# Kernel tuning notes

Measured on AMD Instinct MI355X. Metric: run time of the kernel, lower is better.

The kernel has to match this reference:

```python
import jax, jax.numpy as jnp
import numpy as np
import math

B, S, E, H, F, L, V = 4, 256, 512, 8, 2048, 4, 32000
HD = E // H
MAXLEN = 5000  # EnhancedPositionalEncoding max_len default


def _ln(x, s, b):
    m = jnp.mean(x, axis=-1, keepdims=True)
    v = jnp.mean((x - m) ** 2, axis=-1, keepdims=True)
    return (x - m) / jnp.sqrt(v + 1e-5) * s + b


def setup_inputs() -> dict:
    key = jax.random.key(0)
    ks = jax.random.split(key, 10)
    n = lambda k, shape: jax.random.normal(k, shape, jnp.float32) * 0.02
    return {
        "src": jax.random.randint(ks[0], (B, S), 0, V),
        "emb": jax.random.uniform(ks[1], (V, E), jnp.float32, -0.1, 0.1),
        "rel_table": n(ks[2], (2 * MAXLEN - 1, E)),
        "norm_in_s": jnp.ones(E, jnp.float32), "norm_in_b": jnp.zeros(E, jnp.float32),
        "inW": n(ks[3], (L, 3 * E, E)), "inB": jnp.zeros((L, 3 * E), jnp.float32),
        "outW": n(ks[4], (L, E, E)), "outB": jnp.zeros((L, E), jnp.float32),
        "ln1_s": jnp.ones((L, E), jnp.float32), "ln1_b": jnp.zeros((L, E), jnp.float32),
        "ln2_s": jnp.ones((L, E), jnp.float32), "ln2_b": jnp.zeros((L, E), jnp.float32),
        "w1": n(ks[5], (L, F, E)), "b1": jnp.zeros((L, F), jnp.float32),
        "w2": n(ks[6], (L, E, F)), "b2": jnp.zeros((L, E), jnp.float32),
        "normf_s": jnp.ones(E, jnp.float32), "normf_b": jnp.zeros(E, jnp.float32),
        "dec_w": jax.random.uniform(ks[7], (V, E), jnp.float32, -0.1, 0.1),
        "dec_b": jnp.zeros(V, jnp.float32),
    }


def reference(src, emb, rel_table, norm_in_s, norm_in_b, inW, inB, outW, outB,
              ln1_s, ln1_b, ln2_s, ln2_b, w1, b1, w2, b2, normf_s, normf_b,
              dec_w, dec_b):
    x = emb[src] * math.sqrt(E)                 # [B,S,E], pos_encoder is identity in relative mode
    x = _ln(x, norm_in_s, norm_in_b)
    # relative-position embedding gather: idx[l,m] = (m - l) + S - 1
    pos = jnp.arange(S)
    rel_idx = (pos[None, :] - pos[:, None]) + S - 1
    rel = rel_table[rel_idx].reshape(S, S, H, HD)  # [S,S,H,hd]
    # NOTE: torch adds the BOOL triu mask to float scores -> +1.0 at masked positions
    mask = jnp.triu(jnp.ones((S, S), jnp.float32), 1)
    scale = 1.0 / math.sqrt(HD)
    for l in range(L):
        h = _ln(x, ln1_s[l], ln1_b[l])
        qkv = h @ inW[l].T + inB[l]
        q, k, v = jnp.split(qkv, 3, axis=-1)
        q = q.reshape(B, S, H, HD).transpose(0, 2, 1, 3)  # [B,H,S,hd]
        k = k.reshape(B, S, H, HD).transpose(0, 2, 1, 3)
        v = v.reshape(B, S, H, HD).transpose(0, 2, 1, 3)
        scores = jnp.einsum('bhqd,bhkd->bhqk', q, k) * scale
        bias = jnp.einsum('bhld,lmhd->bhlm', q, rel)      # relative-position bias (unscaled, as in torch)
        attn = jax.nn.softmax(scores + bias + mask, axis=-1)
        o = jnp.einsum('bhqk,bhkd->bhqd', attn, v).transpose(0, 2, 1, 3).reshape(B, S, E)
        x = x + (o @ outW[l].T + outB[l])
        h2 = _ln(x, ln2_s[l], ln2_b[l])
        ff = jax.nn.gelu(h2 @ w1[l].T + b1[l], approximate=False) @ w2[l].T + b2[l]
        x = x + ff
    x = _ln(x, normf_s, normf_b)  # encoder final norm
    return x @ dec_w.T + dec_b    # [B,S,V]
```

## Files before the change

### kernel.cpp

```cpp
#include <hip/hip_runtime.h>
#include <hip/hip_bf16.h>
#include <math.h>

#define BB 4
#define SS 256
#define EE 512
#define HH 8
#define HD 64
#define FFD 2048
#define LL 4
#define VV 32000
#define BS (BB*SS)
#define SQRT_E 22.627416997969522f
#define ATTN_SCALE 0.125f

typedef __bf16 bf16;
typedef __attribute__((ext_vector_type(4))) __bf16 bf16x4;
typedef __attribute__((ext_vector_type(8))) __bf16 bf16x8;
typedef __attribute__((ext_vector_type(4))) float f32x4;

#define GLOBAL_AS __attribute__((address_space(1)))
#define LDS_AS    __attribute__((address_space(3)))

__device__ __forceinline__ void load_lds16(const bf16* g, bf16* l) {
    __builtin_amdgcn_global_load_lds((const GLOBAL_AS unsigned int*)g,
                                     (LDS_AS unsigned int*)l, 16, 0, 0);
}

__global__ void cvt_all(const float* __restrict__ inW, const float* __restrict__ outW,
                        const float* __restrict__ w1, const float* __restrict__ w2,
                        const float* __restrict__ dec, const float* __restrict__ rel,
                        bf16* __restrict__ inWb, bf16* __restrict__ outWb,
                        bf16* __restrict__ w1b, bf16* __restrict__ w2b,
                        bf16* __restrict__ decb, bf16* __restrict__ relb,
                        const int* __restrict__ src, const float* __restrict__ emb,
                        const float* __restrict__ nsc, const float* __restrict__ nbi,
                        float* __restrict__ xout) {
    int b = blockIdx.x;
    int t = threadIdx.x;
    if (b >= 28544) {
        int row = b - 28544;
        const float* r = emb + (size_t)src[row] * EE;
        float v0 = r[t] * SQRT_E, v1 = r[t + 256] * SQRT_E;
        float sum = v0 + v1, sq = v0 * v0 + v1 * v1;
        #pragma unroll
        for (int off = 32; off; off >>= 1) {
            sum += __shfl_xor(sum, off);
            sq  += __shfl_xor(sq, off);
        }
        __shared__ float ssum[4], ssq[4];
        int wid = t >> 6, lane = t & 63;
        if (lane == 0) { ssum[wid] = sum; ssq[wid] = sq; }
        __syncthreads();
        sum = ssum[0] + ssum[1] + ssum[2] + ssum[3];
        sq  = ssq[0] + ssq[1] + ssq[2] + ssq[3];
        float mean = sum * (1.0f / EE);
        float var  = sq * (1.0f / EE) - mean * mean;
        float rstd = rsqrtf(var + 1e-5f);
        xout[(size_t)row * EE + t]       = (v0 - mean) * rstd * nsc[t] + nbi[t];
        xout[(size_t)row * EE + t + 256] = (v1 - mean) * rstd * nsc[t + 256] + nbi[t + 256];
        return;
    }
    const float* s; bf16* d; int base; int n;
    if (b < 3072)       { s = inW;  d = inWb;  base = b;         n = 3145728; }
    else if (b < 4096)  { s = outW; d = outWb; base = b - 3072;  n = 1048576; }
    else if (b < 8192)  { s = w1;   d = w1b;   base = b - 4096;  n = 4194304; }
    else if (b < 12288) { s = w2;   d = w2b;   base = b - 8192;  n = 4194304; }
    else if (b < 28288) { s = dec;  d = decb;  base = b - 12288; n = 16384000; }
    else                { s = rel;  d = relb;  base = b - 28288; n = 261632; }
    int i = (base * 256 + t) * 4;
    if (i < n) {
        float4 v = *(const float4*)(s + i);
        bf16x4 o;
        o[0] = (bf16)v.x; o[1] = (bf16)v.y; o[2] = (bf16)v.z; o[3] = (bf16)v.w;
        *(bf16x4*)(d + i) = o;
    }
}

template <typename OT>
__global__ void ln_kernel(const float* __restrict__ in, const float* __restrict__ sc,
                          const float* __restrict__ bi, OT* __restrict__ out) {
    int row = blockIdx.x;
    int t = threadIdx.x;
    const float* r = in + (size_t)row * EE;
    float v0 = r[t], v1 = r[t + 256];
    float sum = v0 + v1, sq = v0 * v0 + v1 * v1;
    #pragma unroll
    for (int off = 32; off; off >>= 1) {
        sum += __shfl_xor(sum, off);
        sq  += __shfl_xor(sq, off);
    }
    __shared__ float ssum[4], ssq[4];
    int wid = t >> 6, lane = t & 63;
    if (lane == 0) { ssum[wid] = sum; ssq[wid] = sq; }
    __syncthreads();
    sum = ssum[0] + ssum[1] + ssum[2] + ssum[3];
    sq  = ssq[0] + ssq[1] + ssq[2] + ssq[3];
    float mean = sum * (1.0f / EE);
    float var  = sq * (1.0f / EE) - mean * mean;
    float rstd = rsqrtf(var + 1e-5f);
    out[(size_t)row * EE + t]       = (OT)((v0 - mean) * rstd * sc[t] + bi[t]);
    out[(size_t)row * EE + t + 256] = (OT)((v1 - mean) * rstd * sc[t + 256] + bi[t + 256]);
}

__global__ void embed_ln_kernel(const int* __restrict__ src, const float* __restrict__ emb,
                                const float* __restrict__ sc, const float* __restrict__ bi,
                                float* __restrict__ out) {
    int row = blockIdx.x;
    int t = threadIdx.x;
    const float* r = emb + (size_t)src[row] * EE;
    float v0 = r[t] * SQRT_E, v1 = r[t + 256] * SQRT_E;
    float sum = v0 + v1, sq = v0 * v0 + v1 * v1;
    #pragma unroll
    for (int off = 32; off; off >>= 1) {
        sum += __shfl_xor(sum, off);
        sq  += __shfl_xor(sq, off);
    }
    __shared__ float ssum[4], ssq[4];
    int wid = t >> 6, lane = t & 63;
    if (lane == 0) { ssum[wid] = sum; ssq[wid] = sq; }
    __syncthreads();
    sum = ssum[0] + ssum[1] + ssum[2] + ssum[3];
    sq  = ssq[0] + ssq[1] + ssq[2] + ssq[3];
    float mean = sum * (1.0f / EE);
    float var  = sq * (1.0f / EE) - mean * mean;
    float rstd = rsqrtf(var + 1e-5f);
    out[(size_t)row * EE + t]       = (v0 - mean) * rstd * sc[t] + bi[t];
    out[(size_t)row * EE + t + 256] = (v1 - mean) * rstd * sc[t + 256] + bi[t + 256];
}

template <int BM, int BN, int MODE, int OBF16, int WRVT, int SWZ, int SPLITK>
__global__ __launch_bounds__(256) void gemm_bf16(
        const bf16* __restrict__ A, const bf16* __restrict__ W,
        const float* __restrict__ bias, void* __restrict__ Cout,
        const float* __restrict__ res, bf16* __restrict__ vT,
        int M, int N, int K) {
    constexpr int FM = BM / 32, FN = BN / 32;
    __shared__ bf16 Atile[2][BM * 32];
    __shared__ bf16 Btile[2][BN * 32];
    int tid = threadIdx.x;
    int wid = tid >> 6, lane = tid & 63;
    int wm = (wid >> 1) * (BM / 2), wn = (wid & 1) * (BN / 2);
    int bm, bn;
    if (SWZ) {
        int nbm = gridDim.x;
        int linear = blockIdx.y * nbm + blockIdx.x;
        int total = nbm * gridDim.y;
        int chunk = total >> 3;
        int xcd = linear & 7, idx = linear >> 3;
        int g = xcd * chunk + idx;
        bm = (g % nbm) * BM;
        bn = (g / nbm) * BN;
    } else {
        bm = blockIdx.x * BM;
        bn = blockIdx.y * BN;
    }
    int kp = (SPLITK > 1) ? blockIdx.z : 0;
    int kbeg = kp * (K / SPLITK);
    int kend = kbeg + K / SPLITK;

    f32x4 acc[FM][FN];
    #pragma unroll
    for (int i = 0; i < FM; i++)
        #pragma unroll
        for (int j = 0; j < FN; j++)
            acc[i][j] = (f32x4){0.f, 0.f, 0.f, 0.f};

    int mrow = lane & 15, kq = (lane >> 4) * 8;

    auto stage = [&](int buf, int k0) {
        #pragma unroll
        for (int it = 0; it < BM / 64; it++) {
            int c = it * 256 + tid;
            int row = c >> 2, kc = (c & 3) * 8;
            load_lds16(A + (size_t)(bm + row) * K + k0 + kc, &Atile[buf][c * 8]);
        }
        #pragma unroll
        for (int it = 0; it < BN / 64; it++) {
            int c = it * 256 + tid;
            int row = c >> 2, kc = (c & 3) * 8;
            load_lds16(W + (size_t)(bn + row) * K + k0 + kc, &Btile[buf][c * 8]);
        }
    };

    stage(0, kbeg);
    __syncthreads();
    int cur = 0;
    for (int k0 = kbeg; k0 < kend; k0 += 32) {
        if (k0 + 32 < kend) stage(cur ^ 1, k0 + 32);
        bf16x8 af[FM], bfv[FN];
        #pragma unroll
        for (int i = 0; i < FM; i++)
            af[i] = *(const bf16x8*)(&Atile[cur][(wm + i * 16 + mrow) * 32 + kq]);
        #pragma unroll
        for (int j = 0; j < FN; j++)
            bfv[j] = *(const bf16x8*)(&Btile[cur][(wn + j * 16 + mrow) * 32 + kq]);
        #pragma unroll
        for (int i = 0; i < FM; i++)
            #pragma unroll
            for (int j = 0; j < FN; j++)
                acc[i][j] = __builtin_amdgcn_mfma_f32_16x16x32_bf16(af[i], bfv[j], acc[i][j], 0, 0, 0);
        __syncthreads();
        cur ^= 1;
    }

    #pragma unroll
    for (int i = 0; i < FM; i++) {
        int row0 = bm + wm + i * 16 + (lane >> 4) * 4;
        #pragma unroll
        for (int j = 0; j < FN; j++) {
            int col = bn + wn + j * 16 + (lane & 15);
            float bv = bias[col];
            #pragma unroll
            for (int r = 0; r < 4; r++) {
                int row = row0 + r;
                if (SPLITK > 1) {
                    float v = acc[i][j][r];
                    if (kp == 0) v += bv;
                    atomicAdd((float*)Cout + (size_t)row * N + col, v);
                    continue;
                }
                float v = acc[i][j][r] + bv;
                if (MODE == 1) v = 0.5f * v * (1.0f + erff(v * 0.7071067811865476f));
                if (MODE == 2) v += res[(size_t)row * N + col];
                if (WRVT && col >= 1024) {
                    int cc = col - 1024;
                    vT[(size_t)(((row >> 8) * 8 + (cc >> 6)) * 64 + (cc & 63)) * 256 + (row & 255)] = (bf16)v;
                } else if (OBF16) ((bf16*)Cout)[(size_t)row * N + col] = (bf16)v;
                else              ((float*)Cout)[(size_t)row * N + col] = v;
            }
        }
    }
}

__global__ __launch_bounds__(256) void attn_mfma(const bf16* __restrict__ qkv,
        const bf16* __restrict__ relb, const bf16* __restrict__ vT,
        bf16* __restrict__ o) {
    int blk = blockIdx.x;
    int qt = blk & 3, bh = blk >> 2;
    int h = bh & 7, b = bh >> 3;
    int q0 = qt * 64, j0 = 192 - q0;
    int tid = threadIdx.x;
    int wid = tid >> 6, lane = tid & 63;
    int l15 = lane & 15, quad = lane >> 4;
    int mr0 = wid * 16;

    __shared__ __align__(16) bf16 Qs[64 * 72];
    __shared__ __align__(16) bf16 Stg[64 * 72];
    __shared__ __align__(16) bf16 BP[64 * 264];

    int c0 = tid, c1 = 256 + tid;
    int r0 = c0 >> 3, ch0 = (c0 & 7) * 8;
    int r1 = c1 >> 3, ch1 = (c1 & 7) * 8;

    const size_t qbase = (size_t)(b * 256 + q0) * 1536 + h * 64;
    *(bf16x8*)(Qs + r0 * 72 + ch0) = *(const bf16x8*)(qkv + qbase + (size_t)r0 * 1536 + ch0);
    *(bf16x8*)(Qs + r1 * 72 + ch1) = *(const bf16x8*)(qkv + qbase + (size_t)r1 * 1536 + ch1);

    bf16x8 pf0, pf1;
    {
        const size_t rb = (size_t)j0 * 512 + h * 64;
        pf0 = *(const bf16x8*)(relb + rb + (size_t)r0 * 512 + ch0);
        pf1 = *(const bf16x8*)(relb + rb + (size_t)r1 * 512 + ch1);
    }

    __syncthreads();
    bf16x8 af0 = *(const bf16x8*)(Qs + (mr0 + l15) * 72 + quad * 8);
    bf16x8 af1 = *(const bf16x8*)(Qs + (mr0 + l15) * 72 + 32 + quad * 8);

    f32x4 S[16];
    #pragma unroll
    for (int i = 0; i < 16; i++) S[i] = (f32x4){0.f, 0.f, 0.f, 0.f};

    for (int jc = 0; jc < 5; jc++) {
        *(bf16x8*)(Stg + r0 * 72 + ch0) = pf0;
        *(bf16x8*)(Stg + r1 * 72 + ch1) = pf1;
        __syncthreads();
        if (jc < 4) {
            const size_t rb = (size_t)(j0 + (jc + 1) * 64) * 512 + h * 64;
            pf0 = *(const bf16x8*)(relb + rb + (size_t)r0 * 512 + ch0);
            pf1 = *(const bf16x8*)(relb + rb + (size_t)r1 * 512 + ch1);
        } else {
            const size_t kb = (size_t)(b * 256) * 1536 + 512 + h * 64;
            pf0 = *(const bf16x8*)(qkv + kb + (size_t)r0 * 1536 + ch0);
            pf1 = *(const bf16x8*)(qkv + kb + (size_t)r1 * 1536 + ch1);
        }
        #pragma unroll
        for (int jt = 0; jt < 4; jt++) {
            f32x4 acc = (f32x4){0.f, 0.f, 0.f, 0.f};
            bf16x8 bv0 = *(const bf16x8*)(Stg + (jt * 16 + l15) * 72 + quad * 8);
            bf16x8 bv1 = *(const bf16x8*)(Stg + (jt * 16 + l15) * 72 + 32 + quad * 8);
            acc = __builtin_amdgcn_mfma_f32_16x16x32_bf16(af0, bv0, acc, 0, 0, 0);
            acc = __builtin_amdgcn_mfma_f32_16x16x32_bf16(af1, bv1, acc, 0, 0, 0);
            int jp = jc * 64 + jt * 16 + l15;
            #pragma unroll
            for (int r = 0; r < 4; r++) {
                int ll = mr0 + quad * 4 + r;
                int m = jp + ll - 63;
                if (m >= 0 && m < 256) BP[ll * 256 + m] = (bf16)acc[r];
            }
        }
        __syncthreads();
    }

    for (int kc = 0; kc < 4; kc++) {
        *(bf16x8*)(Stg + r0 * 72 + ch0) = pf0;
        *(bf16x8*)(Stg + r1 * 72 + ch1) = pf1;
        __syncthreads();
        if (kc < 3) {
            const size_t kb = (size_t)(b * 256 + (kc + 1) * 64) * 1536 + 512 + h * 64;
            pf0 = *(const bf16x8*)(qkv + kb + (size_t)r0 * 1536 + ch0);
            pf1 = *(const bf16x8*)(qkv + kb + (size_t)r1 * 1536 + ch1);
        } else {
            const size_t vb = (size_t)(bh * 64) * 256;
            pf0 = *(const bf16x8*)(vT + vb + (size_t)r0 * 256 + ch0);
            pf1 = *(const bf16x8*)(vT + vb + (size_t)r1 * 256 + ch1);
        }
        #pragma unroll
        for (int nt = 0; nt < 4; nt++) {
            bf16x8 bv0 = *(const bf16x8*)(Stg + (nt * 16 + l15) * 72 + quad * 8);
            bf16x8 bv1 = *(const bf16x8*)(Stg + (nt * 16 + l15) * 72 + 32 + quad * 8);
            S[kc * 4 + nt] = __builtin_amdgcn_mfma_f32_16x16x32_bf16(af0, bv0, S[kc * 4 + nt], 0, 0, 0);
            S[kc * 4 + nt] = __builtin_amdgcn_mfma_f32_16x16x32_bf16(af1, bv1, S[kc * 4 + nt], 0, 0, 0);
        }
        __syncthreads();
    }

    float rmax[4] = {-1e30f, -1e30f, -1e30f, -1e30f};
    #pragma unroll
    for (int T = 0; T < 16; T++) {
        int m = T * 16 + l15;
        #pragma unroll
        for (int r = 0; r < 4; r++) {
            int ll = mr0 + quad * 4 + r;
            float v = S[T][r] * ATTN_SCALE + (float)BP[ll * 256 + m]
                      + ((m > q0 + ll) ? 1.0f : 0.0f);
            S[T][r] = v;
            rmax[r] = fmaxf(rmax[r], v);
        }
    }
    #pragma unroll
    for (int r = 0; r < 4; r++)
        #pragma unroll
        for (int d = 1; d < 16; d <<= 1)
            rmax[r] = fmaxf(rmax[r], __shfl_xor(rmax[r], d));
    float rsum[4] = {0.f, 0.f, 0.f, 0.f};
    #pragma unroll
    for (int T = 0; T < 16; T++)
        #pragma unroll
        for (int r = 0; r < 4; r++) {
            float p = expf(S[T][r] - rmax[r]);
            S[T][r] = p;
            rsum[r] += p;
        }
    #pragma unroll
    for (int r = 0; r < 4; r++)
        #pragma unroll
        for (int d = 1; d < 16; d <<= 1)
            rsum[r] += __shfl_xor(rsum[r], d);

    __syncthreads();
    #pragma unroll
    for (int T = 0; T < 16; T++)
        #pragma unroll
        for (int r = 0; r < 4; r++)
            BP[(mr0 + quad * 4 + r) * 264 + T * 16 + l15] = (bf16)S[T][r];

    f32x4 oacc[4];
    #pragma unroll
    for (int i = 0; i < 4; i++) oacc[i] = (f32x4){0.f, 0.f, 0.f, 0.f};
    for (int kc = 0; kc < 4; kc++) {
        *(bf16x8*)(Stg + r0 * 72 + ch0) = pf0;
        *(bf16x8*)(Stg + r1 * 72 + ch1) = pf1;
        __syncthreads();
        if (kc < 3) {
            const size_t vb = (size_t)(bh * 64) * 256 + (kc + 1) * 64;
            pf0 = *(const bf16x8*)(vT + vb + (size_t)r0 * 256 + ch0);
            pf1 = *(const bf16x8*)(vT + vb + (size_t)r1 * 256 + ch1);
        }
        #pragma unroll
        for (int ks = 0; ks < 2; ks++) {
            bf16x8 ap = *(const bf16x8*)(BP + (mr0 + l15) * 264 + kc * 64 + ks * 32 + quad * 8);
            #pragma unroll
            for (int nt = 0; nt < 4; nt++) {
                bf16x8 bv = *(const bf16x8*)(Stg + (nt * 16 + l15) * 72 + ks * 32 + quad * 8);
                oacc[nt] = __builtin_amdgcn_mfma_f32_16x16x32_bf16(ap, bv, oacc[nt], 0, 0, 0);
            }
        }
        __syncthreads();
    }

    #pragma unroll
    for (int nt = 0; nt < 4; nt++)
        #pragma unroll
        for (int r = 0; r < 4; r++) {
            int ll = mr0 + quad * 4 + r;
            o[(size_t)(b * 256 + q0 + ll) * 512 + h * 64 + nt * 16 + l15] =
                (bf16)(oacc[nt][r] * (1.0f / rsum[r]));
        }
}

template <int MODE>
__global__ void gemm_nt(const float* __restrict__ A, const float* __restrict__ W,
                        const float* __restrict__ bias, float* __restrict__ C,
                        const float* __restrict__ res, int M, int N, int K) {
    __shared__ float As[64][17];
    __shared__ float Ws[64][17];
    int tid = threadIdx.x;
    int tx = tid & 15, ty = tid >> 4;
    int bm = blockIdx.y * 64, bn = blockIdx.x * 64;
    float acc[4][4] = {};
    for (int k0 = 0; k0 < K; k0 += 16) {
        #pragma unroll
        for (int i = 0; i < 4; i++) {
            int idx = tid + i * 256;
            int r = idx >> 4, c = idx & 15;
            As[r][c] = A[(size_t)(bm + r) * K + k0 + c];
            Ws[r][c] = W[(size_t)(bn + r) * K + k0 + c];
        }
        __syncthreads();
        #pragma unroll
        for (int kk = 0; kk < 16; kk++) {
            float a[4], w[4];
            #pragma unroll
            for (int i = 0; i < 4; i++) a[i] = As[ty * 4 + i][kk];
            #pragma unroll
            for (int j = 0; j < 4; j++) w[j] = Ws[tx * 4 + j][kk];
            #pragma unroll
            for (int i = 0; i < 4; i++)
                #pragma unroll
                for (int j = 0; j < 4; j++)
                    acc[i][j] += a[i] * w[j];
        }
        __syncthreads();
    }
    #pragma unroll
    for (int i = 0; i < 4; i++) {
        int row = bm + ty * 4 + i;
        #pragma unroll
        for (int j = 0; j < 4; j++) {
            int col = bn + tx * 4 + j;
            float v = acc[i][j] + bias[col];
            if (MODE == 1) v = 0.5f * v * (1.0f + erff(v * 0.7071067811865476f));
            if (MODE == 2) v += res[(size_t)row * N + col];
            C[(size_t)row * N + col] = v;
        }
    }
}

__global__ void attn_kernel(const float* __restrict__ qkv, const float* __restrict__ rel_table,
                            float* __restrict__ o) {
    int blk = blockIdx.x;
    int l = blk & (SS - 1);
    int bh = blk >> 8;
    int h = bh & (HH - 1);
    int b = bh >> 3;
    int t = threadIdx.x;
    int wid = t >> 6, lane = t & 63;

    __shared__ float qs[HD];
    __shared__ float attn_s[SS];
    __shared__ float swave[4];
    __shared__ float opart[4][HD];

    const float* qrow = qkv + (size_t)(b * SS + l) * (3 * EE) + h * HD;
    if (t < HD) qs[t] = qrow[t];
    __syncthreads();

    const float* krow   = qkv + (size_t)(b * SS + t) * (3 * EE) + EE + h * HD;
    const float* relrow = rel_table + (size_t)(t - l + SS - 1) * EE + h * HD;
    const float4* k4 = reinterpret_cast<const float4*>(krow);
    const float4* r4 = reinterpret_cast<const float4*>(relrow);
    float s1 = 0.f, s2 = 0.f;
    #pragma unroll
    for (int d4 = 0; d4 < HD / 4; d4++) {
        float4 kv = k4[d4], rv = r4[d4];
        float q0 = qs[4 * d4], q1 = qs[4 * d4 + 1], q2 = qs[4 * d4 + 2], q3 = qs[4 * d4 + 3];
        s1 += q0 * kv.x + q1 * kv.y + q2 * kv.z + q3 * kv.w;
        s2 += q0 * rv.x + q1 * rv.y + q2 * rv.z + q3 * rv.w;
    }
    float val = s1 * ATTN_SCALE + s2 + ((t > l) ? 1.0f : 0.0f);

    float m = val;
    #pragma unroll
    for (int off = 32; off; off >>= 1) m = fmaxf(m, __shfl_xor(m, off));
    if (lane == 0) swave[wid] = m;
    __syncthreads();
    m = fmaxf(fmaxf(swave[0], swave[1]), fmaxf(swave[2], swave[3]));
    float p = expf(val - m);
    float s = p;
    #pragma unroll
    for (int off = 32; off; off >>= 1) s += __shfl_xor(s, off);
    __syncthreads();
    if (lane == 0) swave[wid] = s;
    __syncthreads();
    float tot = swave[0] + swave[1] + swave[2] + swave[3];
    attn_s[t] = p;
    __syncthreads();

    int d = t & 63, part = t >> 6;
    const float* vbase = qkv + (size_t)(b * SS) * (3 * EE) + 2 * EE + h * HD + d;
    float acc = 0.f;
    int m0 = part * 64;
    #pragma unroll 8
    for (int mm = m0; mm < m0 + 64; mm++)
        acc += attn_s[mm] * vbase[(size_t)mm * (3 * EE)];
    opart[part][d] = acc;
    __syncthreads();
    if (t < 64) {
        float ov = (opart[0][d] + opart[1][d] + opart[2][d] + opart[3][d]) / tot;
        o[(size_t)(b * SS + l) * EE + h * HD + d] = ov;
    }
}

extern "C" void kernel_launch(void* const* d_in, const int* in_sizes, int n_in,
                              void* d_out, int out_size, void* d_ws, size_t ws_size,
                              hipStream_t stream) {
    const int*   src    = (const int*)  d_in[0];
    const float* emb    = (const float*)d_in[1];
    const float* rel    = (const float*)d_in[2];
    const float* nin_s  = (const float*)d_in[3];
    const float* nin_b  = (const float*)d_in[4];
    const float* inW    = (const float*)d_in[5];
    const float* inB    = (const float*)d_in[6];
    const float* outW   = (const float*)d_in[7];
    const float* outB   = (const float*)d_in[8];
    const float* ln1_s  = (const float*)d_in[9];
    const float* ln1_b  = (const float*)d_in[10];
    const float* ln2_s  = (const float*)d_in[11];
    const float* ln2_b  = (const float*)d_in[12];
    const float* w1     = (const float*)d_in[13];
    const float* b1     = (const float*)d_in[14];
    const float* w2     = (const float*)d_in[15];
    const float* b2     = (const float*)d_in[16];
    const float* normf_s= (const float*)d_in[17];
    const float* normf_b= (const float*)d_in[18];
    const float* dec_w  = (const float*)d_in[19];
    const float* dec_b  = (const float*)d_in[20];
    float* out = (float*)d_out;

    const size_t n_inW  = (size_t)LL * 3 * EE * EE;
    const size_t n_outW = (size_t)LL * EE * EE;
    const size_t n_w1   = (size_t)LL * FFD * EE;
    const size_t n_w2   = (size_t)LL * EE * FFD;
    const size_t n_dec  = (size_t)VV * EE;

    float* x    = (float*)d_ws;
    bf16*  qkvb = (bf16*)(x + (size_t)BS * EE);
    bf16*  hb   = qkvb + (size_t)BS * 3 * EE;
    bf16*  ob   = hb + (size_t)BS * EE;
    bf16*  ffb  = ob + (size_t)BS * EE;
    bf16*  vTb  = ffb + (size_t)BS * FFD;
    bf16*  relb = vTb + (size_t)BS * 512;
    bf16*  inWb  = relb + (size_t)512 * EE;
    bf16*  outWb = inWb + n_inW;
    bf16*  w1b   = outWb + n_outW;
    bf16*  w2b   = w1b + n_w1;
    bf16*  decWb = w2b + n_w2;
    size_t needed = (size_t)((char*)(decWb + n_dec) - (char*)d_ws);

    if (ws_size >= needed) {
        cvt_all<<<29568, 256, 0, stream>>>(inW, outW, w1, w2, dec_w, rel,
                                           inWb, outWb, w1b, w2b, decWb, relb,
                                           src, emb, nin_s, nin_b, x);

        for (int l = 0; l < LL; l++) {
            ln_kernel<bf16><<<BS, 256, 0, stream>>>(x, ln1_s + l * EE, ln1_b + l * EE, hb);
            gemm_bf16<64, 64, 0, 1, 1, 0, 1><<<dim3(BS / 64, 3 * EE / 64), 256, 0, stream>>>(
                hb, inWb + (size_t)l * 3 * EE * EE, inB + (size_t)l * 3 * EE, qkvb, nullptr,
                vTb, BS, 3 * EE, EE);
            attn_mfma<<<BB * HH * 4, 256, 0, stream>>>(qkvb, relb, vTb, ob);
            gemm_bf16<64, 64, 2, 0, 0, 0, 2><<<dim3(BS / 64, EE / 64, 2), 256, 0, stream>>>(
                ob, outWb + (size_t)l * EE * EE, outB + (size_t)l * EE, x, x,
                nullptr, BS, EE, EE);
            ln_kernel<bf16><<<BS, 256, 0, stream>>>(x, ln2_s + l * EE, ln2_b + l * EE, hb);
            gemm_bf16<64, 64, 1, 1, 0, 0, 1><<<dim3(BS / 64, FFD / 64), 256, 0, stream>>>(
                hb, w1b + (size_t)l * FFD * EE, b1 + (size_t)l * FFD, ffb, nullptr,
                nullptr, BS, FFD, EE);
            gemm_bf16<64, 64, 2, 0, 0, 0, 4><<<dim3(BS / 64, EE / 64, 4), 256, 0, stream>>>(
                ffb, w2b + (size_t)l * EE * FFD, b2 + (size_t)l * EE, x, x,
                nullptr, BS, EE, FFD);
        }

        ln_kernel<bf16><<<BS, 256, 0, stream>>>(x, normf_s, normf_b, hb);
        gemm_bf16<128, 128, 0, 0, 0, 1, 1><<<dim3(BS / 128, VV / 128), 256, 0, stream>>>(
            hb, decWb, dec_b, out, nullptr, nullptr, BS, VV, EE);
    } else {
        float* h     = x + (size_t)BS * EE;
        float* qkvf  = h + (size_t)BS * EE;
        float* o     = qkvf + (size_t)BS * 3 * EE;
        float* ffmid = o + (size_t)BS * EE;

        embed_ln_kernel<<<BS, 256, 0, stream>>>(src, emb, nin_s, nin_b, x);
        for (int l = 0; l < LL; l++) {
            ln_kernel<float><<<BS, 256, 0, stream>>>(x, ln1_s + l * EE, ln1_b + l * EE, h);
            gemm_nt<0><<<dim3(3 * EE / 64, BS / 64), 256, 0, stream>>>(
                h, inW + (size_t)l * 3 * EE * EE, inB + (size_t)l * 3 * EE, qkvf, nullptr,
                BS, 3 * EE, EE);
            attn_kernel<<<BB * HH * SS, 256, 0, stream>>>(qkvf, rel, o);
            gemm_nt<2><<<dim3(EE / 64, BS / 64), 256, 0, stream>>>(
                o, outW + (size_t)l * EE * EE, outB + (size_t)l * EE, x, x,
                BS, EE, EE);
            ln_kernel<float><<<BS, 256, 0, stream>>>(x, ln2_s + l * EE, ln2_b + l * EE, h);
            gemm_nt<1><<<dim3(FFD / 64, BS / 64), 256, 0, stream>>>(
                h, w1 + (size_t)l * FFD * EE, b1 + (size_t)l * FFD, ffmid, nullptr,
                BS, FFD, EE);
            gemm_nt<2><<<dim3(EE / 64, BS / 64), 256, 0, stream>>>(
                ffmid, w2 + (size_t)l * EE * FFD, b2 + (size_t)l * EE, x, x,
                BS, EE, FFD);
        }
        ln_kernel<float><<<BS, 256, 0, stream>>>(x, normf_s, normf_b, h);
        gemm_nt<0><<<dim3(VV / 64, BS / 64), 256, 0, stream>>>(
            h, dec_w, dec_b, out, nullptr, BS, VV, EE);
    }
}
```

Baseline: 577.2 us.

## Fuse encoder layers into one persistent kernel with grid barriers

Replaces the per-layer sequence of LayerNorm, GEMM and attention launches with a single persistent 256-block kernel. The stages are separated by atomic-counter grid barriers, and the barrier counter is reset inside the conversion kernel. LayerNorm is rewritten so each wavefront handles one row with vectorized loads. The goal is to remove about 29 kernel launch gaps and tail effects. The cost is that some stages run on fewer blocks (attention uses only 128 of 256), barrier spin overhead is added, and the kernel depends on all 256 blocks being co-resident.

```diff
diff --git a/kernel.cpp b/kernel.cpp
--- a/kernel.cpp
+++ b/kernel.cpp
@@ -13,6 +13,7 @@
 #define BS (BB*SS)
 #define SQRT_E 22.627416997969522f
 #define ATTN_SCALE 0.125f
+#define NB 256
 
 typedef __bf16 bf16;
 typedef __attribute__((ext_vector_type(4))) __bf16 bf16x4;
@@ -25,6 +26,18 @@
 __device__ __forceinline__ void load_lds16(const bf16* g, bf16* l) {
     __builtin_amdgcn_global_load_lds((const GLOBAL_AS unsigned int*)g,
                                      (LDS_AS unsigned int*)l, 16, 0, 0);
+}
+
+__device__ __forceinline__ void grid_barrier(unsigned* bar, unsigned target) {
+    __syncthreads();
+    if (threadIdx.x == 0) {
+        __threadfence();
+        __hip_atomic_fetch_add(bar, 1u, __ATOMIC_ACQ_REL, __HIP_MEMORY_SCOPE_AGENT);
+        while (__hip_atomic_load(bar, __ATOMIC_ACQUIRE, __HIP_MEMORY_SCOPE_AGENT) < target)
+            __builtin_amdgcn_s_sleep(2);
+        __threadfence();
+    }
+    __syncthreads();
 }
 
 __global__ void cvt_all(const float* __restrict__ inW, const float* __restrict__ outW,
@@ -35,9 +48,10 @@
                         bf16* __restrict__ decb, bf16* __restrict__ relb,
                         const int* __restrict__ src, const float* __restrict__ emb,
                         const float* __restrict__ nsc, const float* __restrict__ nbi,
-                        float* __restrict__ xout) {
+                        float* __restrict__ xout, unsigned* __restrict__ bar) {
     int b = blockIdx.x;
     int t = threadIdx.x;
+    if (b == 0 && t == 0) bar[0] = 0u;
     if (b >= 28544) {
         int row = b - 28544;
         const float* r = emb + (size_t)src[row] * EE;
@@ -129,11 +143,343 @@
     out[(size_t)row * EE + t + 256] = (v1 - mean) * rstd * sc[t + 256] + bi[t + 256];
 }
 
-template <int BM, int BN, int MODE, int OBF16, int WRVT, int SWZ, int SPLITK>
-__global__ __launch_bounds__(256) void gemm_bf16(
+
+__device__ __forceinline__ void ln_wave(const float* __restrict__ in,
+        const float* __restrict__ sc, const float* __restrict__ bi,
+        bf16* __restrict__ out) {
+    int wid = threadIdx.x >> 6, lane = threadIdx.x & 63;
+    int row = blockIdx.x * 4 + wid;
+    const float* r = in + (size_t)row * EE + lane * 8;
+    float4 a = *(const float4*)r;
+    float4 b = *(const float4*)(r + 4);
+    float sum = a.x + a.y + a.z + a.w + b.x + b.y + b.z + b.w;
+    float sq  = a.x*a.x + a.y*a.y + a.z*a.z + a.w*a.w
+              + b.x*b.x + b.y*b.y + b.z*b.z + b.w*b.w;
+    #pragma unroll
+    for (int off = 32; off; off >>= 1) {
+        sum += __shfl_xor(sum, off);
+        sq  += __shfl_xor(sq, off);
+    }
+    float mean = sum * (1.0f / EE);
+    float var  = sq * (1.0f / EE) - mean * mean;
+    float rstd = rsqrtf(var + 1e-5f);
+    float4 s0 = *(const float4*)(sc + lane * 8);
+    float4 s1 = *(const float4*)(sc + lane * 8 + 4);
+    float4 b0 = *(const float4*)(bi + lane * 8);
+    float4 b1 = *(const float4*)(bi + lane * 8 + 4);
+    bf16x8 o;
+    o[0] = (bf16)((a.x - mean) * rstd * s0.x + b0.x);
+    o[1] = (bf16)((a.y - mean) * rstd * s0.y + b0.y);
+    o[2] = (bf16)((a.z - mean) * rstd * s0.z + b0.z);
+    o[3] = (bf16)((a.w - mean) * rstd * s0.w + b0.w);
+    o[4] = (bf16)((b.x - mean) * rstd * s1.x + b1.x);
+    o[5] = (bf16)((b.y - mean) * rstd * s1.y + b1.y);
+    o[6] = (bf16)((b.z - mean) * rstd * s1.z + b1.z);
+    o[7] = (bf16)((b.w - mean) * rstd * s1.w + b1.w);
+    *(bf16x8*)(out + (size_t)row * EE + lane * 8) = o;
+}
+
+template <int MODE, int OBF16, int WRVT, int SPLITK>
+__device__ __forceinline__ void gemm_tile64(
         const bf16* __restrict__ A, const bf16* __restrict__ W,
         const float* __restrict__ bias, void* __restrict__ Cout,
-        const float* __restrict__ res, bf16* __restrict__ vT,
+        bf16* __restrict__ vT, int N, int K,
+        int bm, int bn, int kp, bf16* Asm, bf16* Bsm) {
+    int tid = threadIdx.x;
+    int wid = tid >> 6, lane = tid & 63;
+    int wm = (wid >> 1) * 32, wn = (wid & 1) * 32;
+    int mrow = lane & 15, kq = (lane >> 4) * 8;
+    int kbeg = kp * (K / SPLITK);
+    int kend = kbeg + K / SPLITK;
+
+    f32x4 acc[2][2];
+    #pragma unroll
+    for (int i = 0; i < 2; i++)
+        #pragma unroll
+        for (int j = 0; j < 2; j++)
+            acc[i][j] = (f32x4){0.f, 0.f, 0.f, 0.f};
+
+    auto stage = [&](int buf, int k0) {
+        int row = tid >> 2, kc = (tid & 3) * 8;
+        load_lds16(A + (size_t)(bm + row) * K + k0 + kc, Asm + buf * 2048 + tid * 8);
+        load_lds16(W + (size_t)(bn + row) * K + k0 + kc, Bsm + buf * 2048 + tid * 8);
+    };
+
+    stage(0, kbeg);
+    __syncthreads();
+    int cur = 0;
+    for (int k0 = kbeg; k0 < kend; k0 += 32) {
+        if (k0 + 32 < kend) stage(cur ^ 1, k0 + 32);
+        bf16x8 af[2], bfv[2];
+        #pragma unroll
+        for (int i = 0; i < 2; i++)
+            af[i] = *(const bf16x8*)(Asm + cur * 2048 + (wm + i * 16 + mrow) * 32 + kq);
+        #pragma unroll
+        for (int j = 0; j < 2; j++)
+            bfv[j] = *(const bf16x8*)(Bsm + cur * 2048 + (wn + j * 16 + mrow) * 32 + kq);
+        #pragma unroll
+        for (int i = 0; i < 2; i++)
+            #pragma unroll
+            for (int j = 0; j < 2; j++)
+                acc[i][j] = __builtin_amdgcn_mfma_f32_16x16x32_bf16(af[i], bfv[j], acc[i][j], 0, 0, 0);
+        __syncthreads();
+        cur ^= 1;
+    }
+
+    #pragma unroll
+    for (int i = 0; i < 2; i++) {
+        int row0 = bm + wm + i * 16 + (lane >> 4) * 4;
+        #pragma unroll
+        for (int j = 0; j < 2; j++) {
+            int col = bn + wn + j * 16 + mrow;
+            float bv = bias[col];
+            #pragma unroll
+            for (int r = 0; r < 4; r++) {
+                int row = row0 + r;
+                if (SPLITK > 1) {
+                    float v = acc[i][j][r];
+                    if (kp == 0) v += bv;
+                    atomicAdd((float*)Cout + (size_t)row * N + col, v);
+                } else {
+                    float v = acc[i][j][r] + bv;
+                    if (MODE == 1) v = 0.5f * v * (1.0f + erff(v * 0.7071067811865476f));
+                    if (WRVT && col >= 1024) {
+                        int cc = col - 1024;
+                        vT[(size_t)(((row >> 8) * 8 + (cc >> 6)) * 64 + (cc & 63)) * 256 + (row & 255)] = (bf16)v;
+                    } else if (OBF16) ((bf16*)Cout)[(size_t)row * N + col] = (bf16)v;
+                    else              ((float*)Cout)[(size_t)row * N + col] = v;
+                }
+            }
+        }
+    }
+}
+
+__device__ __forceinline__ void attn_tile(int blk, const bf16* __restrict__ qkv,
+        const bf16* __restrict__ relb, const bf16* __restrict__ vT,
+        bf16* __restrict__ o, bf16* Qs, bf16* Stg, bf16* BP) {
+    int qt = blk & 3, bh = blk >> 2;
+    int h = bh & 7, b = bh >> 3;
+    int q0 = qt * 64, j0 = 192 - q0;
+    int tid = threadIdx.x;
+    int wid = tid >> 6, lane = tid & 63;
+    int l15 = lane & 15, quad = lane >> 4;
+    int mr0 = wid * 16;
+
+    int c0 = tid, c1 = 256 + tid;
+    int r0 = c0 >> 3, ch0 = (c0 & 7) * 8;
+    int r1 = c1 >> 3, ch1 = (c1 & 7) * 8;
+
+    const size_t qbase = (size_t)(b * 256 + q0) * 1536 + h * 64;
+    *(bf16x8*)(Qs + r0 * 72 + ch0) = *(const bf16x8*)(qkv + qbase + (size_t)r0 * 1536 + ch0);
+    *(bf16x8*)(Qs + r1 * 72 + ch1) = *(const bf16x8*)(qkv + qbase + (size_t)r1 * 1536 + ch1);
+
+    bf16x8 pf0, pf1;
+    {
+        const size_t rb = (size_t)j0 * 512 + h * 64;
+        pf0 = *(const bf16x8*)(relb + rb + (size_t)r0 * 512 + ch0);
+        pf1 = *(const bf16x8*)(relb + rb + (size_t)r1 * 512 + ch1);
+    }
+
+    __syncthreads();
+    bf16x8 af0 = *(const bf16x8*)(Qs + (mr0 + l15) * 72 + quad * 8);
+    bf16x8 af1 = *(const bf16x8*)(Qs + (mr0 + l15) * 72 + 32 + quad * 8);
+
+    f32x4 S[16];
+    #pragma unroll
+    for (int i = 0; i < 16; i++) S[i] = (f32x4){0.f, 0.f, 0.f, 0.f};
+
+    for (int jc = 0; jc < 5; jc++) {
+        *(bf16x8*)(Stg + r0 * 72 + ch0) = pf0;
+        *(bf16x8*)(Stg + r1 * 72 + ch1) = pf1;
+        __syncthreads();
+        if (jc < 4) {
+            const size_t rb = (size_t)(j0 + (jc + 1) * 64) * 512 + h * 64;
+            pf0 = *(const bf16x8*)(relb + rb + (size_t)r0 * 512 + ch0);
+            pf1 = *(const bf16x8*)(relb + rb + (size_t)r1 * 512 + ch1);
+        } else {
+            const size_t kb = (size_t)(b * 256) * 1536 + 512 + h * 64;
+            pf0 = *(const bf16x8*)(qkv + kb + (size_t)r0 * 1536 + ch0);
+            pf1 = *(const bf16x8*)(qkv + kb + (size_t)r1 * 1536 + ch1);
+        }
+        #pragma unroll
+        for (int jt = 0; jt < 4; jt++) {
+            f32x4 acc = (f32x4){0.f, 0.f, 0.f, 0.f};
+            bf16x8 bv0 = *(const bf16x8*)(Stg + (jt * 16 + l15) * 72 + quad * 8);
+            bf16x8 bv1 = *(const bf16x8*)(Stg + (jt * 16 + l15) * 72 + 32 + quad * 8);
+            acc = __builtin_amdgcn_mfma_f32_16x16x32_bf16(af0, bv0, acc, 0, 0, 0);
+            acc = __builtin_amdgcn_mfma_f32_16x16x32_bf16(af1, bv1, acc, 0, 0, 0);
+            int jp = jc * 64 + jt * 16 + l15;
+            #pragma unroll
+            for (int r = 0; r < 4; r++) {
+                int ll = mr0 + quad * 4 + r;
+                int m = jp + ll - 63;
+                if (m >= 0 && m < 256) BP[ll * 256 + m] = (bf16)acc[r];
+            }
+        }
+        __syncthreads();
+    }
+
+    for (int kc = 0; kc < 4; kc++) {
+        *(bf16x8*)(Stg + r0 * 72 + ch0) = pf0;
+        *(bf16x8*)(Stg + r1 * 72 + ch1) = pf1;
+        __syncthreads();
+        if (kc < 3) {
+            const size_t kb = (size_t)(b * 256 + (kc + 1) * 64) * 1536 + 512 + h * 64;
+            pf0 = *(const bf16x8*)(qkv + kb + (size_t)r0 * 1536 + ch0);
+            pf1 = *(const bf16x8*)(qkv + kb + (size_t)r1 * 1536 + ch1);
+        } else {
+            const size_t vb = (size_t)(bh * 64) * 256;
+            pf0 = *(const bf16x8*)(vT + vb + (size_t)r0 * 256 + ch0);
+            pf1 = *(const bf16x8*)(vT + vb + (size_t)r1 * 256 + ch1);
+        }
+        #pragma unroll
+        for (int nt = 0; nt < 4; nt++) {
+            bf16x8 bv0 = *(const bf16x8*)(Stg + (nt * 16 + l15) * 72 + quad * 8);
+            bf16x8 bv1 = *(const bf16x8*)(Stg + (nt * 16 + l15) * 72 + 32 + quad * 8);
+            S[kc * 4 + nt] = __builtin_amdgcn_mfma_f32_16x16x32_bf16(af0, bv0, S[kc * 4 + nt], 0, 0, 0);
+            S[kc * 4 + nt] = __builtin_amdgcn_mfma_f32_16x16x32_bf16(af1, bv1, S[kc * 4 + nt], 0, 0, 0);
+        }
+        __syncthreads();
+    }
+
+    float rmax[4] = {-1e30f, -1e30f, -1e30f, -1e30f};
+    #pragma unroll
+    for (int T = 0; T < 16; T++) {
+        int m = T * 16 + l15;
+        #pragma unroll
+        for (int r = 0; r < 4; r++) {
+            int ll = mr0 + quad * 4 + r;
+            float v = S[T][r] * ATTN_SCALE + (float)BP[ll * 256 + m]
+                      + ((m > q0 + ll) ? 1.0f : 0.0f);
+            S[T][r] = v;
+            rmax[r] = fmaxf(rmax[r], v);
+        }
+    }
+    #pragma unroll
+    for (int r = 0; r < 4; r++)
+        #pragma unroll
+        for (int d = 1; d < 16; d <<= 1)
+            rmax[r] = fmaxf(rmax[r], __shfl_xor(rmax[r], d));
+    float rsum[4] = {0.f, 0.f, 0.f, 0.f};
+    #pragma unroll
+    for (int T = 0; T < 16; T++)
+        #pragma unroll
+        for (int r = 0; r < 4; r++) {
+            float p = expf(S[T][r] - rmax[r]);
+            S[T][r] = p;
+            rsum[r] += p;
+        }
+    #pragma unroll
+    for (int r = 0; r < 4; r++)
+        #pragma unroll
+        for (int d = 1; d < 16; d <<= 1)
+            rsum[r] += __shfl_xor(rsum[r], d);
+
+    __syncthreads();
+    #pragma unroll
+    for (int T = 0; T < 16; T++)
+        #pragma unroll
+        for (int r = 0; r < 4; r++)
+            BP[(mr0 + quad * 4 + r) * 264 + T * 16 + l15] = (bf16)S[T][r];
+
+    f32x4 oacc[4];
+    #pragma unroll
+    for (int i = 0; i < 4; i++) oacc[i] = (f32x4){0.f, 0.f, 0.f, 0.f};
+    for (int kc = 0; kc < 4; kc++) {
+        *(bf16x8*)(Stg + r0 * 72 + ch0) = pf0;
+        *(bf16x8*)(Stg + r1 * 72 + ch1) = pf1;
+        __syncthreads();
+        if (kc < 3) {
+            const size_t vb = (size_t)(bh * 64) * 256 + (kc + 1) * 64;
+            pf0 = *(const bf16x8*)(vT + vb + (size_t)r0 * 256 + ch0);
+            pf1 = *(const bf16x8*)(vT + vb + (size_t)r1 * 256 + ch1);
+        }
+        #pragma unroll
+        for (int ks = 0; ks < 2; ks++) {
+            bf16x8 ap = *(const bf16x8*)(BP + (mr0 + l15) * 264 + kc * 64 + ks * 32 + quad * 8);
+            #pragma unroll
+            for (int nt = 0; nt < 4; nt++) {
+                bf16x8 bv = *(const bf16x8*)(Stg + (nt * 16 + l15) * 72 + ks * 32 + quad * 8);
+                oacc[nt] = __builtin_amdgcn_mfma_f32_16x16x32_bf16(ap, bv, oacc[nt], 0, 0, 0);
+            }
+        }
+        __syncthreads();
+    }
+
+    #pragma unroll
+    for (int nt = 0; nt < 4; nt++)
+        #pragma unroll
+        for (int r = 0; r < 4; r++) {
+            int ll = mr0 + quad * 4 + r;
+            o[(size_t)(b * 256 + q0 + ll) * 512 + h * 64 + nt * 16 + l15] =
+                (bf16)(oacc[nt][r] * (1.0f / rsum[r]));
+        }
+}
+
+__global__ __launch_bounds__(256) void encoder_mega(
+        float* __restrict__ x, bf16* __restrict__ hb, bf16* __restrict__ qkvb,
+        bf16* __restrict__ ob, bf16* __restrict__ ffb, bf16* __restrict__ vTb,
+        const bf16* __restrict__ relb,
+        const bf16* __restrict__ inWb, const float* __restrict__ inB,
+        const bf16* __restrict__ outWb, const float* __restrict__ outB,
+        const bf16* __restrict__ w1b, const float* __restrict__ b1,
+        const bf16* __restrict__ w2b, const float* __restrict__ b2,
+        const float* __restrict__ ln1_s, const float* __restrict__ ln1_b,
+        const float* __restrict__ ln2_s, const float* __restrict__ ln2_b,
+        const float* __restrict__ normf_s, const float* __restrict__ normf_b,
+        unsigned* __restrict__ bar) {
+    __shared__ __align__(16) bf16 sQ[64 * 72];
+    __shared__ __align__(16) bf16 sStg[64 * 72];
+    __shared__ __align__(16) bf16 sBP[64 * 264];
+    int blk = blockIdx.x;
+    unsigned tgt = 0;
+
+    #pragma unroll 1
+    for (int l = 0; l < LL; l++) {
+        ln_wave(x, ln1_s + (size_t)l * EE, ln1_b + (size_t)l * EE, hb);
+        tgt += NB; grid_barrier(bar, tgt);
+        for (int job = blk; job < 384; job += NB) {
+            int bm = (job & 15) * 64, bn = (job >> 4) * 64;
+            gemm_tile64<0, 1, 1, 1>(hb, inWb + (size_t)l * 1536 * 512,
+                                    inB + (size_t)l * 1536, qkvb, vTb,
+                                    1536, 512, bm, bn, 0, sQ, sStg);
+        }
+        tgt += NB; grid_barrier(bar, tgt);
+        if (blk < 128) attn_tile(blk, qkvb, relb, vTb, ob, sQ, sStg, sBP);
+        tgt += NB; grid_barrier(bar, tgt);
+        {
+            int kp = blk >> 7, t2 = blk & 127;
+            int bm = (t2 & 15) * 64, bn = (t2 >> 4) * 64;
+            gemm_tile64<2, 0, 0, 2>(ob, outWb + (size_t)l * 512 * 512,
+                                    outB + (size_t)l * 512, x, nullptr,
+                                    512, 512, bm, bn, kp, sQ, sStg);
+        }
+        tgt += NB; grid_barrier(bar, tgt);
+        ln_wave(x, ln2_s + (size_t)l * EE, ln2_b + (size_t)l * EE, hb);
+        tgt += NB; grid_barrier(bar, tgt);
+        for (int job = blk; job < 512; job += NB) {
+            int bm = (job & 15) * 64, bn = (job >> 4) * 64;
+            gemm_tile64<1, 1, 0, 1>(hb, w1b + (size_t)l * 2048 * 512,
+                                    b1 + (size_t)l * 2048, ffb, nullptr,
+                                    2048, 512, bm, bn, 0, sQ, sStg);
+        }
+        tgt += NB; grid_barrier(bar, tgt);
+        for (int job = blk; job < 512; job += NB) {
+            int kp = job >> 7, t2 = job & 127;
+            int bm = (t2 & 15) * 64, bn = (t2 >> 4) * 64;
+            gemm_tile64<2, 0, 0, 4>(ffb, w2b + (size_t)l * 512 * 2048,
+                                    b2 + (size_t)l * 512, x, nullptr,
+                                    512, 2048, bm, bn, kp, sQ, sStg);
+        }
+        tgt += NB; grid_barrier(bar, tgt);
+    }
+    ln_wave(x, normf_s, normf_b, hb);
+}
+
+template <int BM, int BN, int SWZ>
+__global__ __launch_bounds__(256) void gemm_dec(
+        const bf16* __restrict__ A, const bf16* __restrict__ W,
+        const float* __restrict__ bias, float* __restrict__ Cout,
         int M, int N, int K) {
     constexpr int FM = BM / 32, FN = BN / 32;
     __shared__ bf16 Atile[2][BM * 32];
@@ -155,9 +501,6 @@
         bm = blockIdx.x * BM;
         bn = blockIdx.y * BN;
     }
-    int kp = (SPLITK > 1) ? blockIdx.z : 0;
-    int kbeg = kp * (K / SPLITK);
-    int kend = kbeg + K / SPLITK;
 
     f32x4 acc[FM][FN];
     #pragma unroll
@@ -183,11 +526,11 @@
         }
     };
 
-    stage(0, kbeg);
+    stage(0, 0);
     __syncthreads();
     int cur = 0;
-    for (int k0 = kbeg; k0 < kend; k0 += 32) {
-        if (k0 + 32 < kend) stage(cur ^ 1, k0 + 32);
+    for (int k0 = 0; k0 < K; k0 += 32) {
+        if (k0 + 32 < K) stage(cur ^ 1, k0 + 32);
         bf16x8 af[FM], bfv[FN];
         #pragma unroll
         for (int i = 0; i < FM; i++)
@@ -214,190 +557,10 @@
             #pragma unroll
             for (int r = 0; r < 4; r++) {
                 int row = row0 + r;
-                if (SPLITK > 1) {
-                    float v = acc[i][j][r];
-                    if (kp == 0) v += bv;
-                    atomicAdd((float*)Cout + (size_t)row * N + col, v);
-                    continue;
-                }
-                float v = acc[i][j][r] + bv;
-                if (MODE == 1) v = 0.5f * v * (1.0f + erff(v * 0.7071067811865476f));
-                if (MODE == 2) v += res[(size_t)row * N + col];
-                if (WRVT && col >= 1024) {
-                    int cc = col - 1024;
-                    vT[(size_t)(((row >> 8) * 8 + (cc >> 6)) * 64 + (cc & 63)) * 256 + (row & 255)] = (bf16)v;
-                } else if (OBF16) ((bf16*)Cout)[(size_t)row * N + col] = (bf16)v;
-                else              ((float*)Cout)[(size_t)row * N + col] = v;
+                Cout[(size_t)row * N + col] = acc[i][j][r] + bv;
             }
         }
     }
-}
-
-__global__ __launch_bounds__(256) void attn_mfma(const bf16* __restrict__ qkv,
-        const bf16* __restrict__ relb, const bf16* __restrict__ vT,
-        bf16* __restrict__ o) {
-    int blk = blockIdx.x;
-    int qt = blk & 3, bh = blk >> 2;
-    int h = bh & 7, b = bh >> 3;
-    int q0 = qt * 64, j0 = 192 - q0;
-    int tid = threadIdx.x;
-    int wid = tid >> 6, lane = tid & 63;
-    int l15 = lane & 15, quad = lane >> 4;
-    int mr0 = wid * 16;
-
-    __shared__ __align__(16) bf16 Qs[64 * 72];
-    __shared__ __align__(16) bf16 Stg[64 * 72];
-    __shared__ __align__(16) bf16 BP[64 * 264];
-
-    int c0 = tid, c1 = 256 + tid;
-    int r0 = c0 >> 3, ch0 = (c0 & 7) * 8;
-    int r1 = c1 >> 3, ch1 = (c1 & 7) * 8;
-
-    const size_t qbase = (size_t)(b * 256 + q0) * 1536 + h * 64;
-    *(bf16x8*)(Qs + r0 * 72 + ch0) = *(const bf16x8*)(qkv + qbase + (size_t)r0 * 1536 + ch0);
-    *(bf16x8*)(Qs + r1 * 72 + ch1) = *(const bf16x8*)(qkv + qbase + (size_t)r1 * 1536 + ch1);
-
-    bf16x8 pf0, pf1;
-    {
-        const size_t rb = (size_t)j0 * 512 + h * 64;
-        pf0 = *(const bf16x8*)(relb + rb + (size_t)r0 * 512 + ch0);
-        pf1 = *(const bf16x8*)(relb + rb + (size_t)r1 * 512 + ch1);
-    }
-
-    __syncthreads();
-    bf16x8 af0 = *(const bf16x8*)(Qs + (mr0 + l15) * 72 + quad * 8);
-    bf16x8 af1 = *(const bf16x8*)(Qs + (mr0 + l15) * 72 + 32 + quad * 8);
-
-    f32x4 S[16];
-    #pragma unroll
-    for (int i = 0; i < 16; i++) S[i] = (f32x4){0.f, 0.f, 0.f, 0.f};
-
-    for (int jc = 0; jc < 5; jc++) {
-        *(bf16x8*)(Stg + r0 * 72 + ch0) = pf0;
-        *(bf16x8*)(Stg + r1 * 72 + ch1) = pf1;
-        __syncthreads();
-        if (jc < 4) {
-            const size_t rb = (size_t)(j0 + (jc + 1) * 64) * 512 + h * 64;
-            pf0 = *(const bf16x8*)(relb + rb + (size_t)r0 * 512 + ch0);
-            pf1 = *(const bf16x8*)(relb + rb + (size_t)r1 * 512 + ch1);
-        } else {
-            const size_t kb = (size_t)(b * 256) * 1536 + 512 + h * 64;
-            pf0 = *(const bf16x8*)(qkv + kb + (size_t)r0 * 1536 + ch0);
-            pf1 = *(const bf16x8*)(qkv + kb + (size_t)r1 * 1536 + ch1);
-        }
-        #pragma unroll
-        for (int jt = 0; jt < 4; jt++) {
-            f32x4 acc = (f32x4){0.f, 0.f, 0.f, 0.f};
-            bf16x8 bv0 = *(const bf16x8*)(Stg + (jt * 16 + l15) * 72 + quad * 8);
-            bf16x8 bv1 = *(const bf16x8*)(Stg + (jt * 16 + l15) * 72 + 32 + quad * 8);
-            acc = __builtin_amdgcn_mfma_f32_16x16x32_bf16(af0, bv0, acc, 0, 0, 0);
-            acc = __builtin_amdgcn_mfma_f32_16x16x32_bf16(af1, bv1, acc, 0, 0, 0);
-            int jp = jc * 64 + jt * 16 + l15;
-            #pragma unroll
-            for (int r = 0; r < 4; r++) {
-                int ll = mr0 + quad * 4 + r;
-                int m = jp + ll - 63;
-                if (m >= 0 && m < 256) BP[ll * 256 + m] = (bf16)acc[r];
-            }
-        }
-        __syncthreads();
-    }
-
-    for (int kc = 0; kc < 4; kc++) {
-        *(bf16x8*)(Stg + r0 * 72 + ch0) = pf0;
-        *(bf16x8*)(Stg + r1 * 72 + ch1) = pf1;
-        __syncthreads();
-        if (kc < 3) {
-            const size_t kb = (size_t)(b * 256 + (kc + 1) * 64) * 1536 + 512 + h * 64;
-            pf0 = *(const bf16x8*)(qkv + kb + (size_t)r0 * 1536 + ch0);
-            pf1 = *(const bf16x8*)(qkv + kb + (size_t)r1 * 1536 + ch1);
-        } else {
-            const size_t vb = (size_t)(bh * 64) * 256;
-            pf0 = *(const bf16x8*)(vT + vb + (size_t)r0 * 256 + ch0);
-            pf1 = *(const bf16x8*)(vT + vb + (size_t)r1 * 256 + ch1);
-        }
-        #pragma unroll
-        for (int nt = 0; nt < 4; nt++) {
-            bf16x8 bv0 = *(const bf16x8*)(Stg + (nt * 16 + l15) * 72 + quad * 8);
-            bf16x8 bv1 = *(const bf16x8*)(Stg + (nt * 16 + l15) * 72 + 32 + quad * 8);
-            S[kc * 4 + nt] = __builtin_amdgcn_mfma_f32_16x16x32_bf16(af0, bv0, S[kc * 4 + nt], 0, 0, 0);
-            S[kc * 4 + nt] = __builtin_amdgcn_mfma_f32_16x16x32_bf16(af1, bv1, S[kc * 4 + nt], 0, 0, 0);
-        }
-        __syncthreads();
-    }
-
-    float rmax[4] = {-1e30f, -1e30f, -1e30f, -1e30f};
-    #pragma unroll
-    for (int T = 0; T < 16; T++) {
-        int m = T * 16 + l15;
-        #pragma unroll
-        for (int r = 0; r < 4; r++) {
-            int ll = mr0 + quad * 4 + r;
-            float v = S[T][r] * ATTN_SCALE + (float)BP[ll * 256 + m]
-                      + ((m > q0 + ll) ? 1.0f : 0.0f);
-            S[T][r] = v;
-            rmax[r] = fmaxf(rmax[r], v);
-        }
-    }
-    #pragma unroll
-    for (int r = 0; r < 4; r++)
-        #pragma unroll
-        for (int d = 1; d < 16; d <<= 1)
-            rmax[r] = fmaxf(rmax[r], __shfl_xor(rmax[r], d));
-    float rsum[4] = {0.f, 0.f, 0.f, 0.f};
-    #pragma unroll
-    for (int T = 0; T < 16; T++)
-        #pragma unroll
-        for (int r = 0; r < 4; r++) {
-            float p = expf(S[T][r] - rmax[r]);
-            S[T][r] = p;
-            rsum[r] += p;
-        }
-    #pragma unroll
-    for (int r = 0; r < 4; r++)
-        #pragma unroll
-        for (int d = 1; d < 16; d <<= 1)
-            rsum[r] += __shfl_xor(rsum[r], d);
-
-    __syncthreads();
-    #pragma unroll
-    for (int T = 0; T < 16; T++)
-        #pragma unroll
-        for (int r = 0; r < 4; r++)
-            BP[(mr0 + quad * 4 + r) * 264 + T * 16 + l15] = (bf16)S[T][r];
-
-    f32x4 oacc[4];
-    #pragma unroll
-    for (int i = 0; i < 4; i++) oacc[i] = (f32x4){0.f, 0.f, 0.f, 0.f};
-    for (int kc = 0; kc < 4; kc++) {
-        *(bf16x8*)(Stg + r0 * 72 + ch0) = pf0;
-        *(bf16x8*)(Stg + r1 * 72 + ch1) = pf1;
-        __syncthreads();
-        if (kc < 3) {
-            const size_t vb = (size_t)(bh * 64) * 256 + (kc + 1) * 64;
-            pf0 = *(const bf16x8*)(vT + vb + (size_t)r0 * 256 + ch0);
-            pf1 = *(const bf16x8*)(vT + vb + (size_t)r1 * 256 + ch1);
-        }
-        #pragma unroll
-        for (int ks = 0; ks < 2; ks++) {
-            bf16x8 ap = *(const bf16x8*)(BP + (mr0 + l15) * 264 + kc * 64 + ks * 32 + quad * 8);
-            #pragma unroll
-            for (int nt = 0; nt < 4; nt++) {
-                bf16x8 bv = *(const bf16x8*)(Stg + (nt * 16 + l15) * 72 + ks * 32 + quad * 8);
-                oacc[nt] = __builtin_amdgcn_mfma_f32_16x16x32_bf16(ap, bv, oacc[nt], 0, 0, 0);
-            }
-        }
-        __syncthreads();
-    }
-
-    #pragma unroll
-    for (int nt = 0; nt < 4; nt++)
-        #pragma unroll
-        for (int r = 0; r < 4; r++) {
-            int ll = mr0 + quad * 4 + r;
-            o[(size_t)(b * 256 + q0 + ll) * 512 + h * 64 + nt * 16 + l15] =
-                (bf16)(oacc[nt][r] * (1.0f / rsum[r]));
-        }
 }
 
 template <int MODE>
@@ -557,34 +720,21 @@
     bf16*  w1b   = outWb + n_outW;
     bf16*  w2b   = w1b + n_w1;
     bf16*  decWb = w2b + n_w2;
-    size_t needed = (size_t)((char*)(decWb + n_dec) - (char*)d_ws);
+    unsigned* bar = (unsigned*)(decWb + n_dec);
+    size_t needed = (size_t)((char*)(bar + 16) - (char*)d_ws);
 
     if (ws_size >= needed) {
         cvt_all<<<29568, 256, 0, stream>>>(inW, outW, w1, w2, dec_w, rel,
                                            inWb, outWb, w1b, w2b, decWb, relb,
-                                           src, emb, nin_s, nin_b, x);
-
-        for (int l = 0; l < LL; l++) {
-            ln_kernel<bf16><<<BS, 256, 0, stream>>>(x, ln1_s + l * EE, ln1_b + l * EE, hb);
-            gemm_bf16<64, 64, 0, 1, 1, 0, 1><<<dim3(BS / 64, 3 * EE / 64), 256, 0, stream>>>(
-                hb, inWb + (size_t)l * 3 * EE * EE, inB + (size_t)l * 3 * EE, qkvb, nullptr,
-                vTb, BS, 3 * EE, EE);
-            attn_mfma<<<BB * HH * 4, 256, 0, stream>>>(qkvb, relb, vTb, ob);
-            gemm_bf16<64, 64, 2, 0, 0, 0, 2><<<dim3(BS / 64, EE / 64, 2), 256, 0, stream>>>(
-                ob, outWb + (size_t)l * EE * EE, outB + (size_t)l * EE, x, x,
-                nullptr, BS, EE, EE);
-            ln_kernel<bf16><<<BS, 256, 0, stream>>>(x, ln2_s + l * EE, ln2_b + l * EE, hb);
-            gemm_bf16<64, 64, 1, 1, 0, 0, 1><<<dim3(BS / 64, FFD / 64), 256, 0, stream>>>(
-                hb, w1b + (size_t)l * FFD * EE, b1 + (size_t)l * FFD, ffb, nullptr,
-                nullptr, BS, FFD, EE);
-            gemm_bf16<64, 64, 2, 0, 0, 0, 4><<<dim3(BS / 64, EE / 64, 4), 256, 0, stream>>>(
-                ffb, w2b + (size_t)l * EE * FFD, b2 + (size_t)l * EE, x, x,
-                nullptr, BS, EE, FFD);
-        }
-
-        ln_kernel<bf16><<<BS, 256, 0, stream>>>(x, normf_s, normf_b, hb);
-        gemm_bf16<128, 128, 0, 0, 0, 1, 1><<<dim3(BS / 128, VV / 128), 256, 0, stream>>>(
-            hb, decWb, dec_b, out, nullptr, nullptr, BS, VV, EE);
+                                           src, emb, nin_s, nin_b, x, bar);
+
+        encoder_mega<<<NB, 256, 0, stream>>>(
+            x, hb, qkvb, ob, ffb, vTb, relb,
+            inWb, inB, outWb, outB, w1b, b1, w2b, b2,
+            ln1_s, ln1_b, ln2_s, ln2_b, normf_s, normf_b, bar);
+
+        gemm_dec<128, 128, 1><<<dim3(BS / 128, VV / 128), 256, 0, stream>>>(
+            hb, decWb, dec_b, out, BS, VV, EE);
     } else {
         float* h     = x + (size_t)BS * EE;
         float* qkvf  = h + (size_t)BS * EE;
```

Result: slower. 1.389 ms (+140.6%).
